# Optimization experiments

Measured on AMD Instinct MI355X. Metric: run time of the kernel, lower is better.

The kernel has to match this reference:

```python
import jax, jax.numpy as jnp
import numpy as np

B, T, S, V = 128, 8192, 65, 1024  # batch, seq len, states (incl. bookend), obs vocab


def setup_inputs() -> dict:
    key = jax.random.key(0)
    k1, k2, k3 = jax.random.split(key, 3)
    # transition: column 0 (into bookend) forced to -99 pre-softmax, then log_softmax rows
    trans_logits = jax.random.normal(k1, (S, S), dtype=jnp.float32)
    trans_logits = trans_logits.at[:, 0].set(-99.0)
    log_trans = jax.nn.log_softmax(trans_logits, axis=1)
    # categorical emission table, normalized over obs
    log_emit = jax.nn.log_softmax(jax.random.normal(k2, (S, V), dtype=jnp.float32), axis=1)
    # initial distribution: all mass on bookend state 0 (log scale, -99 elsewhere)
    log_pi = jnp.full((S,), -99.0, dtype=jnp.float32).at[0].set(0.0)
    obvs = jax.random.randint(k3, (B, T), 0, V)
    return {"log_trans": log_trans, "log_emit": log_emit, "log_pi": log_pi, "obvs": obvs}


def reference(log_trans, log_emit, log_pi, obvs):
    """Batched HMM log_forward_scan (Durbin Eq. 3.11 + termination).

    Returns log evidence per sequence, shape [B].
    """
    # per-timestep emission log-probs: log_emit[:, obvs] -> [B, T, S] -> [T, B, S]
    em = jnp.transpose(log_emit.T[obvs], (1, 0, 2))

    def step(alpha, em_t):  # alpha: [B, S], em_t: [B, S]
        # alpha'[b, j] = em_t[b, j] + logsumexp_i(alpha[b, i] + log_trans[i, j])
        alpha = jax.nn.logsumexp(alpha[:, :, None] + log_trans[None, :, :], axis=1) + em_t
        return alpha, None

    alpha0 = jnp.broadcast_to(log_pi, (B, S))
    alpha, _ = jax.lax.scan(step, alpha0, em)
    # termination: transition back to bookend state 0
    return jax.nn.logsumexp(alpha + log_trans[None, :, 0], axis=1)
```

## Files before the change

### kernel.cpp

```cpp
#include <hip/hip_runtime.h>
#include <hip/hip_bf16.h>
#include <stdint.h>


#define HMM_B 128
#define HMM_T 8192
#define HMM_S 65
#define HMM_V 1024
#define LN2 0.6931471805599453
#define W_BURN 48
#define NSEG 256
#define SEG_TAIL 16

typedef _Float16 h8 __attribute__((ext_vector_type(8)));
typedef _Float16 h2 __attribute__((ext_vector_type(2)));
typedef int    v4i __attribute__((ext_vector_type(4)));
typedef float  v4f __attribute__((ext_vector_type(4)));
typedef unsigned int uint;
typedef uint   v4u __attribute__((ext_vector_type(4)));

__device__ __attribute__((aligned(16))) __fp16 gETB[4096];
__device__ __attribute__((aligned(16))) __fp16 gEmitHI[HMM_V * 64];
__device__ __attribute__((aligned(16))) float gArowI[64];
__device__ __attribute__((aligned(16))) float gTcsN[64];
__device__ float gTcmax;
__device__ __attribute__((aligned(16))) float gVec[HMM_B * 64];
__device__ __attribute__((aligned(16))) float gLsF[HMM_B * NSEG];

__device__ __forceinline__ void frag_pos(int i, int n, int* r, int* lane, int* j) {
    int t = i >> 5, up = (i >> 4) & 1, g = (i & 15) >> 2, q = i & 3;
    *r = t * 4 + (n >> 4);
    *lane = g * 16 + (n & 15);
    *j = 2 * q + up;
}
__device__ __forceinline__ int ilv_idx(int j) {
    int u = j >> 4, g = (j >> 2) & 3, d = j & 3;
    return g * 16 + (u >> 1) * 8 + d * 2 + (u & 1);
}

__device__ __forceinline__ float fast_rcp(float x) {
#if __has_builtin(__builtin_amdgcn_rcpf)
    return __builtin_amdgcn_rcpf(x);
#else
    return 1.0f / x;
#endif
}
__device__ __forceinline__ h2 h2of(uint u) { return __builtin_bit_cast(h2, u); }
__device__ __forceinline__ uint uof(h2 h) { return __builtin_bit_cast(uint, h); }
__device__ __forceinline__ h2 pk2(float a, float b) {
    return __builtin_bit_cast(h2, __builtin_amdgcn_cvt_pkrtz(a, b));
}
__device__ __forceinline__ int pkh(float a, float b) {
    return __builtin_bit_cast(int, __builtin_amdgcn_cvt_pkrtz(a, b));
}
__device__ __forceinline__ v4f vs(v4f a, float s) {
    return (v4f){a[0] * s, a[1] * s, a[2] * s, a[3] * s};
}

#define MFMA16(A, B, C) __builtin_amdgcn_mfma_f32_16x16x32_f16((A), (B), (C), 0, 0, 0)

#define MFMA_Y                                              \
    {                                                       \
        v4f z4v_ = {0.f, 0.f, 0.f, 0.f};                    \
        v4f D0_ = MFMA16(bfrag_(tET[0]), af0, z4v_);        \
        v4f D1_ = MFMA16(bfrag_(tET[1]), af0, z4v_);        \
        v4f D2_ = MFMA16(bfrag_(tET[2]), af0, z4v_);        \
        v4f D3_ = MFMA16(bfrag_(tET[3]), af0, z4v_);        \
        Y0 = MFMA16(bfrag_(tET[4]), af1, D0_);              \
        Y1 = MFMA16(bfrag_(tET[5]), af1, D1_);              \
        Y2 = MFMA16(bfrag_(tET[6]), af1, D2_);              \
        Y3 = MFMA16(bfrag_(tET[7]), af1, D3_);              \
    }
__device__ __forceinline__ h8 bfrag_(v4i q) { return __builtin_bit_cast(h8, q); }

#define MK_AF(P0, P1, P2, P3, P4, P5, P6, P7)                                         \
    af0 = __builtin_bit_cast(h8, (v4i){(int)uof(P0), (int)uof(P1),                    \
                                       (int)uof(P2), (int)uof(P3)});                  \
    af1 = __builtin_bit_cast(h8, (v4i){(int)uof(P4), (int)uof(P5),                    \
                                       (int)uof(P6), (int)uof(P7)});

#define RENORM_MF(EI)                                                 \
    {                                                                 \
        v4f zz_ = {0.f, 0.f, 0.f, 0.f};                               \
        v4f Sa_ = MFMA16(aones, af0, zz_);                            \
        v4f Sb_ = MFMA16(aones, af1, zz_);                            \
        lsacc -= __log2f(EI);                                         \
        inv = fast_rcp(Sa_[0] + Sb_[0]);                              \
    }

#define APP_F(UA0, UA1, UB0, UB1)                                     \
    {                                                                 \
        float ei_ = inv;                                              \
        h2 iv2_ = pk2(ei_, ei_);                                      \
        h2 e0_ = h2of((UA0)[0]) * iv2_, e1_ = h2of((UA0)[1]) * iv2_;  \
        h2 e2_ = h2of((UA0)[2]) * iv2_, e3_ = h2of((UA0)[3]) * iv2_;  \
        h2 e4_ = h2of((UA1)[0]) * iv2_, e5_ = h2of((UA1)[1]) * iv2_;  \
        h2 e6_ = h2of((UA1)[2]) * iv2_, e7_ = h2of((UA1)[3]) * iv2_;  \
        h2 p0, p1, p2, p3, p4, p5, p6, p7;                            \
        {                                                             \
            v4f Y0, Y1, Y2, Y3;                                       \
            MFMA_Y                                                    \
            p0 = pk2(Y0[0], Y1[0]) * e0_;                             \
            p1 = pk2(Y0[1], Y1[1]) * e1_;                             \
            p2 = pk2(Y0[2], Y1[2]) * e2_;                             \
            p3 = pk2(Y0[3], Y1[3]) * e3_;                             \
            p4 = pk2(Y2[0], Y3[0]) * e4_;                             \
            p5 = pk2(Y2[1], Y3[1]) * e5_;                             \
            p6 = pk2(Y2[2], Y3[2]) * e6_;                             \
            p7 = pk2(Y2[3], Y3[3]) * e7_;                             \
        }                                                             \
        MK_AF(p0, p1, p2, p3, p4, p5, p6, p7)                         \
        {                                                             \
            v4f Y0, Y1, Y2, Y3;                                       \
            MFMA_Y                                                    \
            p0 = pk2(Y0[0], Y1[0]) * h2of((UB0)[0]);                  \
            p1 = pk2(Y0[1], Y1[1]) * h2of((UB0)[1]);                  \
            p2 = pk2(Y0[2], Y1[2]) * h2of((UB0)[2]);                  \
            p3 = pk2(Y0[3], Y1[3]) * h2of((UB0)[3]);                  \
            p4 = pk2(Y2[0], Y3[0]) * h2of((UB1)[0]);                  \
            p5 = pk2(Y2[1], Y3[1]) * h2of((UB1)[1]);                  \
            p6 = pk2(Y2[2], Y3[2]) * h2of((UB1)[2]);                  \
            p7 = pk2(Y2[3], Y3[3]) * h2of((UB1)[3]);                  \
        }                                                             \
        MK_AF(p0, p1, p2, p3, p4, p5, p6, p7)                         \
        RENORM_MF(ei_)                                                \
    }

#define APP_HALF_F(U0, U1)                                            \
    {                                                                 \
        float ei_ = inv;                                              \
        h2 iv2_ = pk2(ei_, ei_);                                      \
        h2 p0, p1, p2, p3, p4, p5, p6, p7;                            \
        {                                                             \
            v4f Y0, Y1, Y2, Y3;                                       \
            MFMA_Y                                                    \
            p0 = pk2(Y0[0], Y1[0]) * (h2of((U0)[0]) * iv2_);          \
            p1 = pk2(Y0[1], Y1[1]) * (h2of((U0)[1]) * iv2_);          \
            p2 = pk2(Y0[2], Y1[2]) * (h2of((U0)[2]) * iv2_);          \
            p3 = pk2(Y0[3], Y1[3]) * (h2of((U0)[3]) * iv2_);          \
            p4 = pk2(Y2[0], Y3[0]) * (h2of((U1)[0]) * iv2_);          \
            p5 = pk2(Y2[1], Y3[1]) * (h2of((U1)[1]) * iv2_);          \
            p6 = pk2(Y2[2], Y3[2]) * (h2of((U1)[2]) * iv2_);          \
            p7 = pk2(Y2[3], Y3[3]) * (h2of((U1)[3]) * iv2_);          \
        }                                                             \
        MK_AF(p0, p1, p2, p3, p4, p5, p6, p7)                         \
        RENORM_MF(ei_)                                                \
    }

#define LDSE_U(U0, U1, U2, U3, W)                                     \
    {                                                                 \
        int vx_ = (W).x, vy_ = (W).y;                                 \
        int bx_ = vx_ << 3, sx_ = vx_ & 7;                            \
        int by_ = vy_ << 3, sy_ = vy_ & 7;                            \
        U0 = ldsU[bx_ + (g2 ^ sx_)];                                  \
        U1 = ldsU[bx_ + ((g2 + 1) ^ sx_)];                            \
        U2 = ldsU[by_ + (g2 ^ sy_)];                                  \
        U3 = ldsU[by_ + ((g2 + 1) ^ sy_)];                            \
    }

#define LDSE_ASM(U0, U1, U2, U3, W)                                               \
    {                                                                             \
        uint vx_ = (uint)(W).x, vy_ = (uint)(W).y;                                \
        uint a0_ = ldsBase + (vx_ << 7) + (((uint)g2 ^ (vx_ & 7u)) << 4);         \
        uint a1_ = a0_ ^ 16u;                                                     \
        uint b0_ = ldsBase + (vy_ << 7) + (((uint)g2 ^ (vy_ & 7u)) << 4);         \
        uint b1_ = b0_ ^ 16u;                                                     \
        asm volatile("ds_read_b128 %0, %4\n\t"                                    \
                     "ds_read_b128 %1, %5\n\t"                                    \
                     "ds_read_b128 %2, %6\n\t"                                    \
                     "ds_read_b128 %3, %7"                                        \
                     : "=&v"(U0), "=&v"(U1), "=&v"(U2), "=&v"(U3)                 \
                     : "v"(a0_), "v"(a1_), "v"(b0_), "v"(b1_)                     \
                     : "memory");                                                 \
    }

#define WAITDS4(U0, U1, U2, U3)                                                   \
    asm volatile("s_waitcnt lgkmcnt(4)"                                           \
                 : "+v"(U0), "+v"(U1), "+v"(U2), "+v"(U3) :: "memory")

__global__ __launch_bounds__(256) void prep_emit(const float* __restrict__ log_emit) {
    int tid = blockIdx.x * 256 + threadIdx.x;
    int v = tid >> 6;
    int j = tid & 63;
    gEmitHI[v * 64 + ilv_idx(j)] = (__fp16)(256.0f * expf(log_emit[(j + 1) * HMM_V + v]));
}

__global__ __launch_bounds__(64) void prep_small(const float* __restrict__ log_trans,
                                                 const float* __restrict__ log_pi) {
    int j = threadIdx.x;
    for (int i = 0; i < 64; ++i) {
        float et = expf(log_trans[(i + 1) * HMM_S + (j + 1)]);
        int r, lane, sj;
        frag_pos(i, j, &r, &lane, &sj);
        gETB[(r * 64 + lane) * 8 + sj] = (__fp16)(et * 16.0f);
    }
    float s = 0.f;
    for (int i = 0; i < HMM_S; ++i)
        s += expf(log_pi[i]) * expf(log_trans[i * HMM_S + (j + 1)]);
    gArowI[ilv_idx(j)] = s;
    float tc = log_trans[(j + 1) * HMM_S + 0];
    float mx = tc;
    for (int d = 1; d < 64; d <<= 1) mx = fmaxf(mx, __shfl_xor(mx, d));
    gTcsN[j] = expf(tc - mx);
    if (j == 0) gTcmax = mx;
}

__global__ __launch_bounds__(512, 1) void hmm_scan(const int* __restrict__ obvs) {
    __shared__ v4u ldsU[HMM_V * 8];

    {
        const v4u* src = (const v4u*)gEmitHI;
        for (int i = threadIdx.x; i < 8192; i += 512) {
            int v = i >> 3, u8 = i & 7;
            ldsU[(v << 3) + (u8 ^ (v & 7))] = src[i];
        }
    }
    __syncthreads();

    const int wid = threadIdx.x >> 6;
    const int lane = threadIdx.x & 63;
    const int task = blockIdx.x * 8 + wid;
    const int bg = task >> 8;
    const int q = task & (NSEG - 1);
    const int g = lane >> 4;
    const int c = lane & 15;
    const int g2 = g * 2;
    const uint ldsBase = (uint)(size_t)(&ldsU[0]);

    const int AstartFull = (q <= 2) ? 0 : SEG_TAIL * q - W_BURN;
    const int* obp = obvs + (size_t)(bg * 16 + c) * HMM_T + (size_t)AstartFull * 2;
    const int g4 = 4 * g;

    v4i tET[8];
    {
        const int4* tb = (const int4*)gETB;
#pragma unroll
        for (int r = 0; r < 8; ++r) {
            int4 t = tb[r * 64 + lane];
            tET[r] = (v4i){t.x, t.y, t.z, t.w};
        }
    }
    h8 aones;
    {
        _Float16 one_ = ((c & 3) == 0) ? (_Float16)1.0f : (_Float16)0.0f;
        aones = (h8){one_, one_, one_, one_, one_, one_, one_, one_};
    }

    float inv = 1.f, lsacc = 0.f;
    h8 af0, af1;

    int kStart, kEnd, burnK;
    if (q <= 2) {
        int2 w0 = *(const int2*)(obp);
        {
            int vx = w0.x, bx = vx << 3, sx = vx & 7;
            v4u I0 = ldsU[bx + (g2 ^ sx)];
            v4u I1 = ldsU[bx + ((g2 + 1) ^ sx)];
            const float* AI = gArowI + g * 16;
            v4f z0, z1, z2, z3;
            {
                h2 ea = h2of(I0[0]), eb = h2of(I0[1]), ec = h2of(I0[2]), ed = h2of(I0[3]);
                z0 = (v4f){AI[0] * (float)ea[0], AI[2] * (float)eb[0],
                           AI[4] * (float)ec[0], AI[6] * (float)ed[0]};
                z1 = (v4f){AI[1] * (float)ea[1], AI[3] * (float)eb[1],
                           AI[5] * (float)ec[1], AI[7] * (float)ed[1]};
                h2 fa = h2of(I1[0]), fb = h2of(I1[1]), fc = h2of(I1[2]), fd = h2of(I1[3]);
                z2 = (v4f){AI[8] * (float)fa[0], AI[10] * (float)fb[0],
                           AI[12] * (float)fc[0], AI[14] * (float)fd[0]};
                z3 = (v4f){AI[9] * (float)fa[1], AI[11] * (float)fb[1],
                           AI[13] * (float)fc[1], AI[15] * (float)fd[1]};
            }
            v4f t_ = (z0 + z1) + (z2 + z3);
            float s_ = (t_[0] + t_[1]) + (t_[2] + t_[3]);
            s_ += __shfl_xor(s_, 16);
            s_ += __shfl_xor(s_, 32);
            float i_ = fast_rcp(s_);
            lsacc = -__log2f(i_);
            z0 = vs(z0, i_); z1 = vs(z1, i_);
            z2 = vs(z2, i_); z3 = vs(z3, i_);
            af0 = __builtin_bit_cast(h8, (v4i){pkh(z0[0], z1[0]), pkh(z0[1], z1[1]),
                                               pkh(z0[2], z1[2]), pkh(z0[3], z1[3])});
            af1 = __builtin_bit_cast(h8, (v4i){pkh(z2[0], z3[0]), pkh(z2[1], z3[1]),
                                               pkh(z2[2], z3[2]), pkh(z2[3], z3[3])});
        }
        {
            int vy = w0.y, by = vy << 3, sy = vy & 7;
            v4u H0 = ldsU[by + (g2 ^ sy)];
            v4u H1 = ldsU[by + ((g2 + 1) ^ sy)];
            APP_HALF_F(H0, H1)
        }
        {
            int2 w1 = *(const int2*)(obp + 2);
            v4u P0, P1, P2, P3;
            LDSE_U(P0, P1, P2, P3, w1)
            APP_F(P0, P1, P2, P3)
        }
        kStart = 2;
        kEnd = SEG_TAIL * (q + 1);
        burnK = (q == 0) ? -1 : SEG_TAIL * q;
    } else {
        const h2 u16 = {(_Float16)0.015625f, (_Float16)0.015625f};
        h2 p0 = u16, p1 = u16, p2 = u16, p3 = u16;
        h2 p4 = u16, p5 = u16, p6 = u16, p7 = u16;
        MK_AF(p0, p1, p2, p3, p4, p5, p6, p7)
        kStart = 0; kEnd = W_BURN + SEG_TAIL; burnK = W_BURN;
    }

    v4u A0, A1, A2, A3, B0, B1, B2, B3;
    int2 wA = *(const int2*)(obp + 2 * kStart);
    int2 wB = *(const int2*)(obp + 2 * (kStart + 1));
    LDSE_ASM(A0, A1, A2, A3, wA)
    LDSE_ASM(B0, B1, B2, B3, wB)
    int2 wC = *(const int2*)(obp + 2 * (kStart + 2 < kEnd ? kStart + 2 : 0));
    int2 wD = *(const int2*)(obp + 2 * (kStart + 3 < kEnd ? kStart + 3 : 0));

    for (int a = kStart; a < kEnd; a += 2) {
        if (a == burnK) {
            lsacc = __log2f(inv);
        }
        WAITDS4(A0, A1, A2, A3);
        APP_F(A0, A1, A2, A3)
        LDSE_ASM(A0, A1, A2, A3, wC)
        wC = *(const int2*)(obp + 2 * (a + 4 < kEnd ? a + 4 : 0));
        WAITDS4(B0, B1, B2, B3);
        APP_F(B0, B1, B2, B3)
        LDSE_ASM(B0, B1, B2, B3, wD)
        wD = *(const int2*)(obp + 2 * (a + 5 < kEnd ? a + 5 : 0));
    }

    if (q != NSEG - 1) {
        lsacc -= __log2f(inv);
    }
    const float subf = (q == 0) ? 380.0f : 384.0f;
    if (lane < 16) {
        gLsF[(bg * 16 + lane) * NSEG + q] = (lsacc - subf) * (float)LN2;
    }
    if (q == NSEG - 1) {
        float* vp = gVec + (size_t)(bg * 16 + c) * 64 + g4;
        *(v4f*)(vp)      = (v4f){(float)af0[0], (float)af0[2], (float)af0[4], (float)af0[6]};
        *(v4f*)(vp + 16) = (v4f){(float)af0[1], (float)af0[3], (float)af0[5], (float)af0[7]};
        *(v4f*)(vp + 32) = (v4f){(float)af1[0], (float)af1[2], (float)af1[4], (float)af1[6]};
        *(v4f*)(vp + 48) = (v4f){(float)af1[1], (float)af1[3], (float)af1[5], (float)af1[7]};
    }
}

__global__ __launch_bounds__(64) void hmm_combine(float* __restrict__ out) {
    const int b = blockIdx.x;
    const int lane = threadIdx.x;
    float pr = gVec[b * 64 + lane] * gTcsN[lane];
#pragma unroll
    for (int d = 1; d < 64; d <<= 1) pr += __shfl_xor(pr, d);
    double acc = 0.0;
    for (int k = lane; k < NSEG; k += 64) acc += (double)gLsF[b * NSEG + k];
#pragma unroll
    for (int d = 1; d < 64; d <<= 1) acc += __shfl_xor(acc, d);
    if (lane == 0) {
        out[b] = (float)(acc + (double)gTcmax + log((double)pr));
    }
}

extern "C" void kernel_launch(void* const* d_in, const int* in_sizes, int n_in,
                              void* d_out, int out_size, void* d_ws, size_t ws_size,
                              hipStream_t stream) {
    const float* log_trans = (const float*)d_in[0];
    const float* log_emit  = (const float*)d_in[1];
    const float* log_pi    = (const float*)d_in[2];
    const int*   obvs      = (const int*)d_in[3];
    float* out = (float*)d_out;

    prep_emit<<<256, 256, 0, stream>>>(log_emit);
    prep_small<<<1, 64, 0, stream>>>(log_trans, log_pi);
    hmm_scan<<<256, 512, 0, stream>>>(obvs);
    hmm_combine<<<HMM_B, 64, 0, stream>>>(out);
}
```

Before: 114.2 us.

## Merge prep kernels and fold combine into scan via atomics and completion counter

```diff
diff --git a/kernel.cpp b/kernel.cpp
--- a/kernel.cpp
+++ b/kernel.cpp
@@ -24,8 +24,8 @@
 __device__ __attribute__((aligned(16))) float gArowI[64];
 __device__ __attribute__((aligned(16))) float gTcsN[64];
 __device__ float gTcmax;
-__device__ __attribute__((aligned(16))) float gVec[HMM_B * 64];
-__device__ __attribute__((aligned(16))) float gLsF[HMM_B * NSEG];
+__device__ __attribute__((aligned(16))) double gAcc[HMM_B];
+__device__ __attribute__((aligned(16))) uint gDone[8];
 
 __device__ __forceinline__ void frag_pos(int i, int n, int* r, int* lane, int* j) {
     int t = i >> 5, up = (i >> 4) & 1, g = (i & 15) >> 2, q = i & 3;
@@ -178,34 +178,45 @@
     asm volatile("s_waitcnt lgkmcnt(4)"                                           \
                  : "+v"(U0), "+v"(U1), "+v"(U2), "+v"(U3) :: "memory")
 
-__global__ __launch_bounds__(256) void prep_emit(const float* __restrict__ log_emit) {
-    int tid = blockIdx.x * 256 + threadIdx.x;
-    int v = tid >> 6;
-    int j = tid & 63;
-    gEmitHI[v * 64 + ilv_idx(j)] = (__fp16)(256.0f * expf(log_emit[(j + 1) * HMM_V + v]));
-}
-
-__global__ __launch_bounds__(64) void prep_small(const float* __restrict__ log_trans,
-                                                 const float* __restrict__ log_pi) {
-    int j = threadIdx.x;
-    for (int i = 0; i < 64; ++i) {
-        float et = expf(log_trans[(i + 1) * HMM_S + (j + 1)]);
-        int r, lane, sj;
-        frag_pos(i, j, &r, &lane, &sj);
-        gETB[(r * 64 + lane) * 8 + sj] = (__fp16)(et * 16.0f);
-    }
-    float s = 0.f;
-    for (int i = 0; i < HMM_S; ++i)
-        s += expf(log_pi[i]) * expf(log_trans[i * HMM_S + (j + 1)]);
-    gArowI[ilv_idx(j)] = s;
-    float tc = log_trans[(j + 1) * HMM_S + 0];
-    float mx = tc;
-    for (int d = 1; d < 64; d <<= 1) mx = fmaxf(mx, __shfl_xor(mx, d));
-    gTcsN[j] = expf(tc - mx);
-    if (j == 0) gTcmax = mx;
-}
-
-__global__ __launch_bounds__(512, 1) void hmm_scan(const int* __restrict__ obvs) {
+__global__ __launch_bounds__(256) void prep(const float* __restrict__ log_emit,
+                                            const float* __restrict__ log_trans,
+                                            const float* __restrict__ log_pi) {
+    int b = blockIdx.x;
+    if (b < 256) {
+        int tid = b * 256 + threadIdx.x;
+        int v = tid >> 6;
+        int j = tid & 63;
+        gEmitHI[v * 64 + ilv_idx(j)] =
+            (__fp16)(256.0f * expf(log_emit[(j + 1) * HMM_V + v]));
+        return;
+    }
+    int t = threadIdx.x;
+    if (t < 64) {
+        int j = t;
+        for (int i = 0; i < 64; ++i) {
+            float et = expf(log_trans[(i + 1) * HMM_S + (j + 1)]);
+            int r, lane, sj;
+            frag_pos(i, j, &r, &lane, &sj);
+            gETB[(r * 64 + lane) * 8 + sj] = (__fp16)(et * 16.0f);
+        }
+        float s = 0.f;
+        for (int i = 0; i < HMM_S; ++i)
+            s += expf(log_pi[i]) * expf(log_trans[i * HMM_S + (j + 1)]);
+        gArowI[ilv_idx(j)] = s;
+        float tc = log_trans[(j + 1) * HMM_S + 0];
+        float mx = tc;
+        for (int d = 1; d < 64; d <<= 1) mx = fmaxf(mx, __shfl_xor(mx, d));
+        gTcsN[j] = expf(tc - mx);
+        if (j == 0) gTcmax = mx;
+    } else if (t < 64 + HMM_B) {
+        gAcc[t - 64] = 0.0;
+    } else if (t < 64 + HMM_B + 8) {
+        gDone[t - 64 - HMM_B] = 0u;
+    }
+}
+
+__global__ __launch_bounds__(512, 1) void hmm_scan(const int* __restrict__ obvs,
+                                                   float* __restrict__ out) {
     __shared__ v4u ldsU[HMM_V * 8];
 
     {
@@ -333,29 +344,33 @@
     }
     const float subf = (q == 0) ? 380.0f : 384.0f;
     if (lane < 16) {
-        gLsF[(bg * 16 + lane) * NSEG + q] = (lsacc - subf) * (float)LN2;
-    }
+        atomicAdd(&gAcc[bg * 16 + lane], (double)((lsacc - subf) * (float)LN2));
+    }
+    __threadfence();
+    if (lane == 0) atomicAdd(&gDone[bg], 1u);
+
     if (q == NSEG - 1) {
-        float* vp = gVec + (size_t)(bg * 16 + c) * 64 + g4;
-        *(v4f*)(vp)      = (v4f){(float)af0[0], (float)af0[2], (float)af0[4], (float)af0[6]};
-        *(v4f*)(vp + 16) = (v4f){(float)af0[1], (float)af0[3], (float)af0[5], (float)af0[7]};
-        *(v4f*)(vp + 32) = (v4f){(float)af1[0], (float)af1[2], (float)af1[4], (float)af1[6]};
-        *(v4f*)(vp + 48) = (v4f){(float)af1[1], (float)af1[3], (float)af1[5], (float)af1[7]};
-    }
-}
-
-__global__ __launch_bounds__(64) void hmm_combine(float* __restrict__ out) {
-    const int b = blockIdx.x;
-    const int lane = threadIdx.x;
-    float pr = gVec[b * 64 + lane] * gTcsN[lane];
+        float pr = 0.f;
+        const float* T = gTcsN;
 #pragma unroll
-    for (int d = 1; d < 64; d <<= 1) pr += __shfl_xor(pr, d);
-    double acc = 0.0;
-    for (int k = lane; k < NSEG; k += 64) acc += (double)gLsF[b * NSEG + k];
-#pragma unroll
-    for (int d = 1; d < 64; d <<= 1) acc += __shfl_xor(acc, d);
-    if (lane == 0) {
-        out[b] = (float)(acc + (double)gTcmax + log((double)pr));
+        for (int d = 0; d < 4; ++d) {
+            pr += (float)af0[2 * d]     * T[g4 + d]
+                + (float)af0[2 * d + 1] * T[16 + g4 + d]
+                + (float)af1[2 * d]     * T[32 + g4 + d]
+                + (float)af1[2 * d + 1] * T[48 + g4 + d];
+        }
+        pr += __shfl_xor(pr, 16);
+        pr += __shfl_xor(pr, 32);
+        while (__hip_atomic_load(&gDone[bg], __ATOMIC_RELAXED,
+                                 __HIP_MEMORY_SCOPE_AGENT) < NSEG) {
+            __builtin_amdgcn_s_sleep(8);
+        }
+        __threadfence();
+        if (lane < 16) {
+            double acc = __hip_atomic_load(&gAcc[bg * 16 + lane], __ATOMIC_RELAXED,
+                                           __HIP_MEMORY_SCOPE_AGENT);
+            out[bg * 16 + lane] = (float)(acc + (double)gTcmax + log((double)pr));
+        }
     }
 }
 
@@ -368,8 +383,6 @@
     const int*   obvs      = (const int*)d_in[3];
     float* out = (float*)d_out;
 
-    prep_emit<<<256, 256, 0, stream>>>(log_emit);
-    prep_small<<<1, 64, 0, stream>>>(log_trans, log_pi);
-    hmm_scan<<<256, 512, 0, stream>>>(obvs);
-    hmm_combine<<<HMM_B, 64, 0, stream>>>(out);
-}
+    prep<<<257, 256, 0, stream>>>(log_emit, log_trans, log_pi);
+    hmm_scan<<<256, 512, 0, stream>>>(obvs, out);
+}
```

Result: slower. 143.2 us (+25.4%).
